# Optimization experiments

Hardware: AMD Instinct MI355X
Metric: run time of the kernel (lower is better)

## Reference

```python
import jax, jax.numpy as jnp
import numpy as np

N_HEAD = 16

def setup_inputs() -> dict:
    key = jax.random.key(0)
    k1, k2, k3 = jax.random.split(key, 3)
    B, T, E = 4, 2048, 1024
    x = jax.random.normal(k1, (B, T, E), dtype=jnp.float32)
    w_attn = jax.random.normal(k2, (4 * E, E), dtype=jnp.float32) * (1.0 / np.sqrt(E))
    b_attn = jax.random.normal(k3, (4 * E,), dtype=jnp.float32) * 0.02
    return {"x": x, "w_attn": w_attn, "b_attn": b_attn}

def reference(x, w_attn, b_attn):
    B, T, C = x.shape
    H = N_HEAD
    D = C // H  # head_dim
    qkv = x @ w_attn.T + b_attn                      # [B,T,4C]
    q, k, v = qkv[..., :C], qkv[..., C:2*C], qkv[..., 2*C:3*C]  # 4th chunk unused
    q = q.reshape(B, T, H, D).transpose(0, 2, 1, 3)  # [B,H,T,D]
    k = k.reshape(B, T, H, D).transpose(0, 2, 1, 3)
    v = v.reshape(B, T, H, D).transpose(0, 2, 1, 3)
    scale = 1.0 / np.sqrt(D)
    attn = jnp.einsum('bhqd,bhkd->bhqk', q, k) * scale  # [B,H,T,T]
    causal = jnp.tril(jnp.ones((T, T), dtype=bool))
    attn = jnp.where(causal[None, None], attn, -jnp.inf)
    attn = jax.nn.softmax(attn, axis=-1)
    y = jnp.einsum('bhqk,bhkd->bhqd', attn, v)       # [B,H,T,D]
    return y.transpose(0, 2, 1, 3).reshape(B, T, C)
```

## Files before the change

### kernel.cpp

```cpp
#include <hip/hip_runtime.h>
#include <math.h>


using short8 = __attribute__((ext_vector_type(8))) short;
using f32x4  = __attribute__((ext_vector_type(4))) float;

__device__ __forceinline__ ushort f2bf(float f) {
    union { float f; unsigned u; } x{f};
    unsigned r = x.u + 0x7fffu + ((x.u >> 16) & 1u);
    return (ushort)(r >> 16);
}
__device__ __forceinline__ unsigned pack_bf16_ru(float a, float b) {
    union { float f; unsigned u; } x{a}, y{b};
    return __builtin_amdgcn_perm(y.u + 0x8000u, x.u + 0x8000u, 0x07060302u);
}

__device__ __forceinline__ void gload_lds16(const void* g, void* l) {
    __builtin_amdgcn_global_load_lds(
        (const __attribute__((address_space(1))) void*)g,
        (__attribute__((address_space(3))) void*)l, 16, 0, 0);
}

__global__ void cvt_all(const float* __restrict__ x, const float* __restrict__ w,
                        ushort* __restrict__ xb, ushort* __restrict__ wb) {
    int i = blockIdx.x * blockDim.x + threadIdx.x;
    const float* src; ushort* dst; int j;
    if (i < 2097152) { src = x; dst = xb; j = i; }
    else             { src = w; dst = wb; j = i - 2097152; if (j >= 786432) return; }
    float4 v = ((const float4*)src)[j];
    ushort4 o;
    o.x = f2bf(v.x); o.y = f2bf(v.y); o.z = f2bf(v.z); o.w = f2bf(v.w);
    ((ushort4*)dst)[j] = o;
}

__global__ __launch_bounds__(256) void qkv_gemm(
    const ushort* __restrict__ A, const ushort* __restrict__ W,
    const float* __restrict__ bias,
    ushort* __restrict__ Qo, ushort* __restrict__ Ko, ushort* __restrict__ Vt)
{
    __shared__ ushort As[128 * 64];
    __shared__ ushort Ws[128 * 64];
    const int id = (int)blockIdx.x;
    const int xcd = id & 7, s = id >> 3;
    const int bm = xcd * 8 + (s & 7);
    const int bn = s >> 3;
    const int tid = threadIdx.x;
    const int wave = tid >> 6, lane = tid & 63;
    const int quad = lane >> 4, l16 = lane & 15, l7 = l16 & 7;
    const int wm = (wave >> 1) * 64, wn = (wave & 1) * 64;

    const ushort* Abase = A + (size_t)(bm * 128) * 1024;
    const ushort* Wbase = W + (size_t)(bn * 128) * 1024;

    f32x4 acc[4][4];
#pragma unroll
    for (int i = 0; i < 4; i++)
#pragma unroll
        for (int j = 0; j < 4; j++) acc[i][j] = (f32x4){0.f, 0.f, 0.f, 0.f};

    for (int k0 = 0; k0 < 1024; k0 += 64) {
        __syncthreads();
#pragma unroll
        for (int j = 0; j < 4; j++) {
            const int rb = wave * 32 + j * 8;
            const int r  = rb + (lane >> 3);
            const int cc = (lane & 7) ^ (r & 7);
            gload_lds16(Abase + (size_t)r * 1024 + k0 + cc * 8, &As[rb * 64]);
            gload_lds16(Wbase + (size_t)r * 1024 + k0 + cc * 8, &Ws[rb * 64]);
        }
        __syncthreads();
        short8 af[4][2], wf[4][2];
#pragma unroll
        for (int t = 0; t < 4; t++)
#pragma unroll
            for (int kg = 0; kg < 2; kg++) {
                const int pc = ((kg * 4 + quad) ^ l7) * 8;
                af[t][kg] = *(const short8*)&As[(wm + t * 16 + l16) * 64 + pc];
                wf[t][kg] = *(const short8*)&Ws[(wn + t * 16 + l16) * 64 + pc];
            }
#pragma unroll
        for (int kg = 0; kg < 2; kg++)
#pragma unroll
            for (int tm = 0; tm < 4; tm++)
#pragma unroll
                for (int tn = 0; tn < 4; tn++)
                    acc[tm][tn] = __builtin_amdgcn_mfma_f32_16x16x32_bf16(af[tm][kg], wf[tn][kg], acc[tm][tn], 0, 0, 0);
    }

    const float SCALE_Q = 0.125f * 1.4426950408889634f;
#pragma unroll
    for (int tn = 0; tn < 4; tn++) {
        const int n = bn * 128 + wn + tn * 16 + l16;
        const float bv = bias[n];
#pragma unroll
        for (int tm = 0; tm < 4; tm++) {
            const int m0 = bm * 128 + wm + tm * 16 + quad * 4;
            const int b0 = m0 >> 11, t0 = m0 & 2047;
            if (n < 1024) {
                const int h = n >> 6, d = n & 63;
#pragma unroll
                for (int r = 0; r < 4; r++)
                    Qo[((size_t)(b0 * 16 + h) * 2048 + t0 + r) * 64 + d] = f2bf((acc[tm][tn][r] + bv) * SCALE_Q);
            } else if (n < 2048) {
                const int c = n - 1024, h = c >> 6, d = c & 63;
#pragma unroll
                for (int r = 0; r < 4; r++)
                    Ko[((size_t)(b0 * 16 + h) * 2048 + t0 + r) * 64 + d] = f2bf(acc[tm][tn][r] + bv);
            } else {
                const int c = n - 2048, h = c >> 6, d = c & 63;
                uint2 pk;
                pk.x = pack_bf16_ru(acc[tm][tn][0] + bv, acc[tm][tn][1] + bv);
                pk.y = pack_bf16_ru(acc[tm][tn][2] + bv, acc[tm][tn][3] + bv);
                *(uint2*)&Vt[((size_t)(b0 * 16 + h) * 64 + d) * 2048 + t0] = pk;
            }
        }
    }
}

__global__ __launch_bounds__(256) void attn_fwd(
    const ushort* __restrict__ Q, const ushort* __restrict__ K,
    const ushort* __restrict__ Vt, float* __restrict__ out)
{
    __shared__ ushort Ks[2][64 * 64];
    __shared__ ushort Vs[2][64 * 64];
    __shared__ ushort Ps[4][16 * 64];
    const int id = (int)blockIdx.x;
    const int bh = id & 63;
    const int s  = id >> 6;
    const int g = s >> 2, r4 = s & 3;
    const int qt = (g == 0) ? 15 - r4 : (g == 1) ? 8 + r4 : (g == 2) ? 7 - r4 : r4;
    const int b = bh >> 4, h = bh & 15;
    const int wave = threadIdx.x >> 6, lane = threadIdx.x & 63;
    const int quad = lane >> 4, l16 = lane & 15, l7 = l16 & 7;

    const ushort* Kbh = K  + (size_t)bh * 2048 * 64;
    const ushort* Vbh = Vt + (size_t)bh * 64 * 2048;
    ushort* Pw = Ps[wave];

    int qb[2];
    qb[0] = qt * 128 + wave * 16;
    qb[1] = qb[0] + 64;

    short8 qf[2][2];
#pragma unroll
    for (int qg = 0; qg < 2; qg++) {
        const ushort* Qp = Q + ((size_t)bh * 2048 + qb[qg] + l16) * 64;
        qf[qg][0] = *(const short8*)(Qp + quad * 8);
        qf[qg][1] = *(const short8*)(Qp + 32 + quad * 8);
    }

    f32x4 o[2][4];
#pragma unroll
    for (int qg = 0; qg < 2; qg++)
#pragma unroll
        for (int dg = 0; dg < 4; dg++) o[qg][dg] = (f32x4){0.f, 0.f, 0.f, 0.f};
    float lsum[2] = {0.f, 0.f};

    const int ntiles = 2 * qt + 2;

#define STAGE(k0_, bf_)                                                              \
    {                                                                                \
        _Pragma("unroll")                                                            \
        for (int j = 0; j < 2; j++) {                                                \
            const int rb = wave * 16 + j * 8;                                        \
            const int r  = rb + (lane >> 3);                                         \
            const int cc = (lane & 7) ^ (r & 7);                                     \
            gload_lds16(Kbh + (size_t)((k0_) + r) * 64 + cc * 8, &Ks[bf_][rb * 64]); \
            gload_lds16(Vbh + (size_t)r * 2048 + (k0_) + cc * 8, &Vs[bf_][rb * 64]); \
        }                                                                            \
    }

    STAGE(0, 0);
    int buf = 0, k0 = 0;
    for (int it = 0; it < ntiles; ++it, k0 += 64, buf ^= 1) {
        __syncthreads();
        if (it + 1 < ntiles) STAGE(k0 + 64, buf ^ 1);
        if (k0 > qb[1] + 15) continue;

        const bool act0 = k0 <= qb[0] + 15;

        short8 kf[4][2];
#pragma unroll
        for (int t = 0; t < 4; t++)
#pragma unroll
            for (int dh = 0; dh < 2; dh++)
                kf[t][dh] = *(const short8*)&Ks[buf][(t * 16 + l16) * 64 + (((dh * 4 + quad) ^ l7) * 8)];
        short8 vf[2][4];
#pragma unroll
        for (int kg = 0; kg < 2; kg++) {
            const int pc = ((kg * 4 + quad) ^ l7) * 8;
#pragma unroll
            for (int dg = 0; dg < 4; dg++)
                vf[kg][dg] = *(const short8*)&Vs[buf][(dg * 16 + l16) * 64 + pc];
        }

#pragma unroll
        for (int qg = 0; qg < 2; qg++) {
            if (qg == 0 && !act0) continue;
            f32x4 sc[4];
            __builtin_amdgcn_s_setprio(1);
#pragma unroll
            for (int t = 0; t < 4; t++) {
                f32x4 z = (f32x4){0.f, 0.f, 0.f, 0.f};
                z = __builtin_amdgcn_mfma_f32_16x16x32_bf16(kf[t][0], qf[qg][0], z, 0, 0, 0);
                z = __builtin_amdgcn_mfma_f32_16x16x32_bf16(kf[t][1], qf[qg][1], z, 0, 0, 0);
                sc[t] = z;
            }
            __builtin_amdgcn_s_setprio(0);
            const int q = qb[qg] + l16;
            float p[16];
            if (k0 + 63 > qb[qg]) {
#pragma unroll
                for (int t = 0; t < 4; t++)
#pragma unroll
                    for (int r = 0; r < 4; r++) {
                        const int key = k0 + t * 16 + quad * 4 + r;
                        const float sv = (key <= q) ? sc[t][r] : -INFINITY;
                        p[t * 4 + r] = __builtin_amdgcn_exp2f(sv);
                    }
            } else {
#pragma unroll
                for (int t = 0; t < 4; t++)
#pragma unroll
                    for (int r = 0; r < 4; r++)
                        p[t * 4 + r] = __builtin_amdgcn_exp2f(sc[t][r]);
            }
            {
                const float s0 = (p[0] + p[1]) + (p[2] + p[3]);
                const float s1 = (p[4] + p[5]) + (p[6] + p[7]);
                const float s2 = (p[8] + p[9]) + (p[10] + p[11]);
                const float s3 = (p[12] + p[13]) + (p[14] + p[15]);
                lsum[qg] += (s0 + s1) + (s2 + s3);
            }
#pragma unroll
            for (int t = 0; t < 4; t++) {
                uint2 pk;
                pk.x = pack_bf16_ru(p[t * 4 + 0], p[t * 4 + 1]);
                pk.y = pack_bf16_ru(p[t * 4 + 2], p[t * 4 + 3]);
                const int pc = ((2 * t + (quad >> 1)) ^ l7) * 8 + (quad & 1) * 4;
                *(uint2*)(Pw + l16 * 64 + pc) = pk;
            }
#pragma unroll
            for (int kg = 0; kg < 2; kg++) {
                short8 pf = *(const short8*)(Pw + l16 * 64 + (((kg * 4 + quad) ^ l7) * 8));
                __builtin_amdgcn_s_setprio(1);
#pragma unroll
                for (int dg = 0; dg < 4; dg++)
                    o[qg][dg] = __builtin_amdgcn_mfma_f32_16x16x32_bf16(vf[kg][dg], pf, o[qg][dg], 0, 0, 0);
                __builtin_amdgcn_s_setprio(0);
            }
        }
    }
#undef STAGE

#pragma unroll
    for (int qg = 0; qg < 2; qg++) {
        float l = lsum[qg];
        l += __shfl_xor(l, 16);
        l += __shfl_xor(l, 32);
        const float rinv = 1.f / l;
        float* op = out + ((size_t)(b * 2048 + qb[qg] + l16)) * 1024 + h * 64;
#pragma unroll
        for (int dg = 0; dg < 4; dg++) {
            float4 v;
            v.x = o[qg][dg][0] * rinv; v.y = o[qg][dg][1] * rinv;
            v.z = o[qg][dg][2] * rinv; v.w = o[qg][dg][3] * rinv;
            *(float4*)(op + dg * 16 + quad * 4) = v;
        }
    }
}

extern "C" void kernel_launch(void* const* d_in, const int* in_sizes, int n_in,
                              void* d_out, int out_size, void* d_ws, size_t ws_size,
                              hipStream_t stream) {
    const float* x    = (const float*)d_in[0];
    const float* w    = (const float*)d_in[1];
    const float* bias = (const float*)d_in[2];

    ushort* xb  = (ushort*)d_ws;
    ushort* wb  = xb + 8388608;
    ushort* Qb  = wb + 3145728;
    ushort* Kb  = Qb + 8388608;
    ushort* Vtb = Kb + 8388608;

    cvt_all<<<11264, 256, 0, stream>>>(x, w, xb, wb);
    qkv_gemm<<<1536, 256, 0, stream>>>(xb, wb, bias, Qb, Kb, Vtb);
    attn_fwd<<<1024, 256, 0, stream>>>(Qb, Kb, Vtb, (float*)d_out);
}
```

Before: 227.4 us.

## Pair complementary 64-row query tiles per block for uniform causal work

Each attention block now processes two 64-row query tiles, pr and 31-pr, one after the other in a single 33-iteration loop over key tiles. Every block therefore does the same amount of work, replacing the old scheme of 128-row tiles with hand-ordered scheduling. The aim is to remove load imbalance and tail effects across the grid. In exchange, each staged K/V tile now feeds only one 64-row query group instead of two, so reuse of K/V loads and LDS fragments drops. The runtime-indexed ph into qf, o and lsum may also cost extra registers or selects, and the s_setprio hints were removed.

```diff
diff --git a/kernel.cpp b/kernel.cpp
--- a/kernel.cpp
+++ b/kernel.cpp
@@ -126,9 +126,9 @@
     __shared__ ushort Ps[4][16 * 64];
     const int id = (int)blockIdx.x;
     const int bh = id & 63;
-    const int s  = id >> 6;
-    const int g = s >> 2, r4 = s & 3;
-    const int qt = (g == 0) ? 15 - r4 : (g == 1) ? 8 + r4 : (g == 2) ? 7 - r4 : r4;
+    const int pr = id >> 6;
+    const int qtA = pr, qtB = 31 - pr;
+    const int na = qtA + 1;
     const int b = bh >> 4, h = bh & 15;
     const int wave = threadIdx.x >> 6, lane = threadIdx.x & 63;
     const int quad = lane >> 4, l16 = lane & 15, l7 = l16 & 7;
@@ -138,25 +138,23 @@
     ushort* Pw = Ps[wave];
 
     int qb[2];
-    qb[0] = qt * 128 + wave * 16;
-    qb[1] = qb[0] + 64;
+    qb[0] = qtA * 64 + wave * 16;
+    qb[1] = qtB * 64 + wave * 16;
 
     short8 qf[2][2];
 #pragma unroll
-    for (int qg = 0; qg < 2; qg++) {
-        const ushort* Qp = Q + ((size_t)bh * 2048 + qb[qg] + l16) * 64;
-        qf[qg][0] = *(const short8*)(Qp + quad * 8);
-        qf[qg][1] = *(const short8*)(Qp + 32 + quad * 8);
+    for (int ph = 0; ph < 2; ph++) {
+        const ushort* Qp = Q + ((size_t)bh * 2048 + qb[ph] + l16) * 64;
+        qf[ph][0] = *(const short8*)(Qp + quad * 8);
+        qf[ph][1] = *(const short8*)(Qp + 32 + quad * 8);
     }
 
     f32x4 o[2][4];
 #pragma unroll
-    for (int qg = 0; qg < 2; qg++)
-#pragma unroll
-        for (int dg = 0; dg < 4; dg++) o[qg][dg] = (f32x4){0.f, 0.f, 0.f, 0.f};
+    for (int ph = 0; ph < 2; ph++)
+#pragma unroll
+        for (int dg = 0; dg < 4; dg++) o[ph][dg] = (f32x4){0.f, 0.f, 0.f, 0.f};
     float lsum[2] = {0.f, 0.f};
-
-    const int ntiles = 2 * qt + 2;
 
 #define STAGE(k0_, bf_)                                                              \
     {                                                                                \
@@ -171,13 +169,16 @@
     }
 
     STAGE(0, 0);
-    int buf = 0, k0 = 0;
-    for (int it = 0; it < ntiles; ++it, k0 += 64, buf ^= 1) {
+    int buf = 0;
+    for (int i = 0; i < 33; ++i, buf ^= 1) {
+        const int ph = (i >= na) ? 1 : 0;
+        const int k0 = ((ph ? i - na : i)) * 64;
         __syncthreads();
-        if (it + 1 < ntiles) STAGE(k0 + 64, buf ^ 1);
-        if (k0 > qb[1] + 15) continue;
-
-        const bool act0 = k0 <= qb[0] + 15;
+        if (i + 1 < 33) {
+            const int j = i + 1;
+            const int nk0 = ((j >= na) ? j - na : j) * 64;
+            STAGE(nk0, buf ^ 1);
+        }
 
         short8 kf[4][2];
 #pragma unroll
@@ -194,77 +195,69 @@
                 vf[kg][dg] = *(const short8*)&Vs[buf][(dg * 16 + l16) * 64 + pc];
         }
 
-#pragma unroll
-        for (int qg = 0; qg < 2; qg++) {
-            if (qg == 0 && !act0) continue;
-            f32x4 sc[4];
-            __builtin_amdgcn_s_setprio(1);
-#pragma unroll
-            for (int t = 0; t < 4; t++) {
-                f32x4 z = (f32x4){0.f, 0.f, 0.f, 0.f};
-                z = __builtin_amdgcn_mfma_f32_16x16x32_bf16(kf[t][0], qf[qg][0], z, 0, 0, 0);
-                z = __builtin_amdgcn_mfma_f32_16x16x32_bf16(kf[t][1], qf[qg][1], z, 0, 0, 0);
-                sc[t] = z;
-            }
-            __builtin_amdgcn_s_setprio(0);
-            const int q = qb[qg] + l16;
-            float p[16];
-            if (k0 + 63 > qb[qg]) {
-#pragma unroll
-                for (int t = 0; t < 4; t++)
-#pragma unroll
-                    for (int r = 0; r < 4; r++) {
-                        const int key = k0 + t * 16 + quad * 4 + r;
-                        const float sv = (key <= q) ? sc[t][r] : -INFINITY;
-                        p[t * 4 + r] = __builtin_amdgcn_exp2f(sv);
-                    }
-            } else {
-#pragma unroll
-                for (int t = 0; t < 4; t++)
-#pragma unroll
-                    for (int r = 0; r < 4; r++)
-                        p[t * 4 + r] = __builtin_amdgcn_exp2f(sc[t][r]);
-            }
-            {
-                const float s0 = (p[0] + p[1]) + (p[2] + p[3]);
-                const float s1 = (p[4] + p[5]) + (p[6] + p[7]);
-                const float s2 = (p[8] + p[9]) + (p[10] + p[11]);
-                const float s3 = (p[12] + p[13]) + (p[14] + p[15]);
-                lsum[qg] += (s0 + s1) + (s2 + s3);
-            }
-#pragma unroll
-            for (int t = 0; t < 4; t++) {
-                uint2 pk;
-                pk.x = pack_bf16_ru(p[t * 4 + 0], p[t * 4 + 1]);
-                pk.y = pack_bf16_ru(p[t * 4 + 2], p[t * 4 + 3]);
-                const int pc = ((2 * t + (quad >> 1)) ^ l7) * 8 + (quad & 1) * 4;
-                *(uint2*)(Pw + l16 * 64 + pc) = pk;
-            }
-#pragma unroll
-            for (int kg = 0; kg < 2; kg++) {
-                short8 pf = *(const short8*)(Pw + l16 * 64 + (((kg * 4 + quad) ^ l7) * 8));
-                __builtin_amdgcn_s_setprio(1);
-#pragma unroll
-                for (int dg = 0; dg < 4; dg++)
-                    o[qg][dg] = __builtin_amdgcn_mfma_f32_16x16x32_bf16(vf[kg][dg], pf, o[qg][dg], 0, 0, 0);
-                __builtin_amdgcn_s_setprio(0);
-            }
+        f32x4 sc[4];
+#pragma unroll
+        for (int t = 0; t < 4; t++) {
+            f32x4 z = (f32x4){0.f, 0.f, 0.f, 0.f};
+            z = __builtin_amdgcn_mfma_f32_16x16x32_bf16(kf[t][0], qf[ph][0], z, 0, 0, 0);
+            z = __builtin_amdgcn_mfma_f32_16x16x32_bf16(kf[t][1], qf[ph][1], z, 0, 0, 0);
+            sc[t] = z;
+        }
+        const int q = qb[ph] + l16;
+        float p[16];
+        if (k0 + 63 > qb[ph]) {
+#pragma unroll
+            for (int t = 0; t < 4; t++)
+#pragma unroll
+                for (int r = 0; r < 4; r++) {
+                    const int key = k0 + t * 16 + quad * 4 + r;
+                    const float sv = (key <= q) ? sc[t][r] : -INFINITY;
+                    p[t * 4 + r] = __builtin_amdgcn_exp2f(sv);
+                }
+        } else {
+#pragma unroll
+            for (int t = 0; t < 4; t++)
+#pragma unroll
+                for (int r = 0; r < 4; r++)
+                    p[t * 4 + r] = __builtin_amdgcn_exp2f(sc[t][r]);
+        }
+        {
+            const float s0 = (p[0] + p[1]) + (p[2] + p[3]);
+            const float s1 = (p[4] + p[5]) + (p[6] + p[7]);
+            const float s2 = (p[8] + p[9]) + (p[10] + p[11]);
+            const float s3 = (p[12] + p[13]) + (p[14] + p[15]);
+            lsum[ph] += (s0 + s1) + (s2 + s3);
+        }
+#pragma unroll
+        for (int t = 0; t < 4; t++) {
+            uint2 pk;
+            pk.x = pack_bf16_ru(p[t * 4 + 0], p[t * 4 + 1]);
+            pk.y = pack_bf16_ru(p[t * 4 + 2], p[t * 4 + 3]);
+            const int pc = ((2 * t + (quad >> 1)) ^ l7) * 8 + (quad & 1) * 4;
+            *(uint2*)(Pw + l16 * 64 + pc) = pk;
+        }
+#pragma unroll
+        for (int kg = 0; kg < 2; kg++) {
+            short8 pf = *(const short8*)(Pw + l16 * 64 + (((kg * 4 + quad) ^ l7) * 8));
+#pragma unroll
+            for (int dg = 0; dg < 4; dg++)
+                o[ph][dg] = __builtin_amdgcn_mfma_f32_16x16x32_bf16(vf[kg][dg], pf, o[ph][dg], 0, 0, 0);
         }
     }
 #undef STAGE
 
 #pragma unroll
-    for (int qg = 0; qg < 2; qg++) {
-        float l = lsum[qg];
+    for (int ph = 0; ph < 2; ph++) {
+        float l = lsum[ph];
         l += __shfl_xor(l, 16);
         l += __shfl_xor(l, 32);
         const float rinv = 1.f / l;
-        float* op = out + ((size_t)(b * 2048 + qb[qg] + l16)) * 1024 + h * 64;
+        float* op = out + ((size_t)(b * 2048 + qb[ph] + l16)) * 1024 + h * 64;
 #pragma unroll
         for (int dg = 0; dg < 4; dg++) {
             float4 v;
-            v.x = o[qg][dg][0] * rinv; v.y = o[qg][dg][1] * rinv;
-            v.z = o[qg][dg][2] * rinv; v.w = o[qg][dg][3] * rinv;
+            v.x = o[ph][dg][0] * rinv; v.y = o[ph][dg][1] * rinv;
+            v.z = o[ph][dg][2] * rinv; v.w = o[ph][dg][3] * rinv;
             *(float4*)(op + dg * 16 + quad * 4) = v;
         }
     }
```

New measurement: 468.2 us. 2.06x slower.

## Load K/V fragments directly from global memory instead of double-buffered LDS

Applied to the files above, without the earlier changes.

Removes the shared-memory K and V double buffers, the async global-to-LDS staging and the per-tile __syncthreads. Each wave now reads its K and V MFMA fragments straight from global memory, and the s_setprio hints around the MFMAs are dropped. The aim is to remove block-wide barriers and LDS traffic and to free LDS for occupancy. In exchange, each of the four waves reloads the same K/V tiles from global memory or cache, and global latency is no longer hidden by prefetching.

```diff
diff --git a/kernel.cpp b/kernel.cpp
--- a/kernel.cpp
+++ b/kernel.cpp
@@ -121,8 +121,6 @@
     const ushort* __restrict__ Q, const ushort* __restrict__ K,
     const ushort* __restrict__ Vt, float* __restrict__ out)
 {
-    __shared__ ushort Ks[2][64 * 64];
-    __shared__ ushort Vs[2][64 * 64];
     __shared__ ushort Ps[4][16 * 64];
     const int id = (int)blockIdx.x;
     const int bh = id & 63;
@@ -158,25 +156,8 @@
 
     const int ntiles = 2 * qt + 2;
 
-#define STAGE(k0_, bf_)                                                              \
-    {                                                                                \
-        _Pragma("unroll")                                                            \
-        for (int j = 0; j < 2; j++) {                                                \
-            const int rb = wave * 16 + j * 8;                                        \
-            const int r  = rb + (lane >> 3);                                         \
-            const int cc = (lane & 7) ^ (r & 7);                                     \
-            gload_lds16(Kbh + (size_t)((k0_) + r) * 64 + cc * 8, &Ks[bf_][rb * 64]); \
-            gload_lds16(Vbh + (size_t)r * 2048 + (k0_) + cc * 8, &Vs[bf_][rb * 64]); \
-        }                                                                            \
-    }
-
-    STAGE(0, 0);
-    int buf = 0, k0 = 0;
-    for (int it = 0; it < ntiles; ++it, k0 += 64, buf ^= 1) {
-        __syncthreads();
-        if (it + 1 < ntiles) STAGE(k0 + 64, buf ^ 1);
-        if (k0 > qb[1] + 15) continue;
-
+    for (int it = 0; it < ntiles; ++it) {
+        const int k0 = it * 64;
         const bool act0 = k0 <= qb[0] + 15;
 
         short8 kf[4][2];
@@ -184,21 +165,18 @@
         for (int t = 0; t < 4; t++)
 #pragma unroll
             for (int dh = 0; dh < 2; dh++)
-                kf[t][dh] = *(const short8*)&Ks[buf][(t * 16 + l16) * 64 + (((dh * 4 + quad) ^ l7) * 8)];
+                kf[t][dh] = *(const short8*)(Kbh + (size_t)(k0 + t * 16 + l16) * 64 + dh * 32 + quad * 8);
         short8 vf[2][4];
 #pragma unroll
-        for (int kg = 0; kg < 2; kg++) {
-            const int pc = ((kg * 4 + quad) ^ l7) * 8;
+        for (int kg = 0; kg < 2; kg++)
 #pragma unroll
             for (int dg = 0; dg < 4; dg++)
-                vf[kg][dg] = *(const short8*)&Vs[buf][(dg * 16 + l16) * 64 + pc];
-        }
+                vf[kg][dg] = *(const short8*)(Vbh + (size_t)(dg * 16 + l16) * 2048 + k0 + kg * 32 + quad * 8);
 
 #pragma unroll
         for (int qg = 0; qg < 2; qg++) {
             if (qg == 0 && !act0) continue;
             f32x4 sc[4];
-            __builtin_amdgcn_s_setprio(1);
 #pragma unroll
             for (int t = 0; t < 4; t++) {
                 f32x4 z = (f32x4){0.f, 0.f, 0.f, 0.f};
@@ -206,7 +184,6 @@
                 z = __builtin_amdgcn_mfma_f32_16x16x32_bf16(kf[t][1], qf[qg][1], z, 0, 0, 0);
                 sc[t] = z;
             }
-            __builtin_amdgcn_s_setprio(0);
             const int q = qb[qg] + l16;
             float p[16];
             if (k0 + 63 > qb[qg]) {
@@ -243,15 +220,12 @@
 #pragma unroll
             for (int kg = 0; kg < 2; kg++) {
                 short8 pf = *(const short8*)(Pw + l16 * 64 + (((kg * 4 + quad) ^ l7) * 8));
-                __builtin_amdgcn_s_setprio(1);
 #pragma unroll
                 for (int dg = 0; dg < 4; dg++)
                     o[qg][dg] = __builtin_amdgcn_mfma_f32_16x16x32_bf16(vf[kg][dg], pf, o[qg][dg], 0, 0, 0);
-                __builtin_amdgcn_s_setprio(0);
-            }
-        }
-    }
-#undef STAGE
+            }
+        }
+    }
 
 #pragma unroll
     for (int qg = 0; qg < 2; qg++) {
```

Measured after the change: 295.2 us. 1.3x slower.
